# Kernel tuning notes

Hardware: AMD Instinct MI355X
Metric: run time of the kernel (lower is better)

The kernel has to match this reference:

```python
import jax, jax.numpy as jnp
import numpy as np

TAU = 1.2  # relaxed-categorical temperature (forward default)


def setup_inputs() -> dict:
    key = jax.random.key(0)
    ks = jax.random.split(key, 8)
    B, F, V, E, H, T = 1024, 2048, 4096, 256, 1024, 32
    n = lambda k, shape: jax.random.normal(k, shape, jnp.float32) * 0.1
    return {
        "t": jax.random.normal(ks[0], (B, F), jnp.float32),
        "embedding": n(ks[1], (V, E)),
        "aff_w": n(ks[2], (H, F)),
        "aff_b": jnp.zeros((H,), jnp.float32),
        "w_ih": n(ks[3], (4 * H, E)),
        "w_hh": n(ks[4], (4 * H, H)),
        "b_ih": jnp.zeros((4 * H,), jnp.float32),
        # PyTorch init: forget-gate bias (second quarter) set to 1
        "b_hh": jnp.zeros((4 * H,), jnp.float32).at[H:2 * H].set(1.0),
        "lp_w": n(ks[5], (V, H)),
        "lp_b": jnp.zeros((V,), jnp.float32),
        "start_token_idx": 1,
        "max_sentence_length": T,
    }


def reference(t, embedding, aff_w, aff_b, w_ih, w_hh, b_ih, b_hh, lp_w, lp_b,
              start_token_idx, max_sentence_length):
    B = t.shape[0]
    H = aff_w.shape[0]
    V = embedding.shape[0]

    h0 = t @ aff_w.T + aff_b                      # [B, H]
    c0 = jnp.zeros((B, H), t.dtype)
    tok0 = jax.nn.one_hot(jnp.full((B,), start_token_idx), V, dtype=t.dtype)

    # Gumbel noise for RelaxedOneHotCategorical rsample, one slab per step
    gumbel = jax.random.gumbel(jax.random.key(42), (max_sentence_length, B, V), t.dtype)

    def step(carry, g):
        h, c, tok = carry
        emb = tok @ embedding                     # [B, E] (one-hot/relaxed matmul)
        gates = emb @ w_ih.T + b_ih + h @ w_hh.T + b_hh  # [B, 4H]
        i, f, gg, o = jnp.split(gates, 4, axis=-1)        # PyTorch gate order i,f,g,o
        c = jax.nn.sigmoid(f) * c + jax.nn.sigmoid(i) * jnp.tanh(gg)
        h = jax.nn.sigmoid(o) * jnp.tanh(c)
        # softmax probs -> relaxed sample: softmax((log p + G)/tau)
        logp = jax.nn.log_softmax(h @ lp_w.T + lp_b, axis=-1)  # [B, V]
        y = jax.nn.softmax((logp + g) / TAU, axis=-1)
        hard = jax.nn.one_hot(jnp.argmax(y, axis=-1), V, dtype=y.dtype)
        tok = jax.lax.stop_gradient(hard - y) + y  # straight-through
        return (h, c, tok), tok

    _, toks = jax.lax.scan(step, (h0, c0, tok0), gumbel)  # toks: [T, B, V]
    message = jnp.concatenate([tok0[None], toks], axis=0)  # [T+1, B, V]
    return jnp.transpose(message, (1, 0, 2))               # [B, T+1, V]
```

## Files before the change

kernel.cpp:

```cpp
#include <hip/hip_runtime.h>
#include <math.h>


typedef _Float16 f16;
typedef f16 f16x8 __attribute__((ext_vector_type(8)));
typedef float f32x4 __attribute__((ext_vector_type(4)));

#define F16_MIN_NORM 6.104e-5f

__device__ __forceinline__ void split_f16(float v, f16& h, f16& l) {
  f16 h0 = (fabsf(v) < F16_MIN_NORM) ? (f16)0.0f : (f16)v;
  float r = (v - (float)h0) * 4096.0f;
  h = h0; l = (f16)r;
}

__device__ __forceinline__ float sigm(float x) { return 1.0f / (1.0f + expf(-x)); }

#define GLOAD_LDS16(gsrc, ldst)                                               \
  __builtin_amdgcn_global_load_lds(                                           \
      (const __attribute__((address_space(1))) unsigned int*)(const void*)(gsrc), \
      (__attribute__((address_space(3))) unsigned int*)(void*)(ldst), 16, 0, 0)


__device__ __forceinline__ unsigned tf_rotl(unsigned x, int r) {
  return (x << r) | (x >> (32 - r));
}

__device__ inline float gumbel_at(unsigned idx) {
  const unsigned ks0 = 0u;
  const unsigned ks1 = 42u;
  const unsigned ks2 = 0x1BD11BDAu ^ ks0 ^ ks1;
  unsigned x0 = 0u + ks0;
  unsigned x1 = idx + ks1;
#define TFR(rot) { x0 += x1; x1 = tf_rotl(x1, rot); x1 ^= x0; }
  TFR(13) TFR(15) TFR(26) TFR(6)
  x0 += ks1; x1 += ks2 + 1u;
  TFR(17) TFR(29) TFR(16) TFR(24)
  x0 += ks2; x1 += ks0 + 2u;
  TFR(13) TFR(15) TFR(26) TFR(6)
  x0 += ks0; x1 += ks1 + 3u;
  TFR(17) TFR(29) TFR(16) TFR(24)
  x0 += ks1; x1 += ks2 + 4u;
  TFR(13) TFR(15) TFR(26) TFR(6)
  x0 += ks2; x1 += ks0 + 5u;
#undef TFR
  const unsigned bits = x0 ^ x1;
  const float f = __uint_as_float((bits >> 9) | 0x3F800000u) - 1.0f;
  const float tiny = 1.17549435082228751e-38f;
  const float u = fmaxf(tiny, f * (1.0f - tiny) + tiny);
  return -logf(-logf(u));
}


__global__ void init_kernel(float* __restrict__ out, const int* __restrict__ startp,
                            int* __restrict__ tok, int Tp1, int V) {
  const int b = blockIdx.x;
  const int start = *startp;
  if (threadIdx.x == 0) tok[b] = start;
  float* orow = out + (size_t)b * Tp1 * V;
  const int tq = start >> 2;
  for (int v4 = threadIdx.x; v4 < V / 4; v4 += blockDim.x) {
    float4 v = make_float4(0.f, 0.f, 0.f, 0.f);
    if (v4 == tq) ((float*)&v)[start & 3] = 1.0f;
    ((float4*)orow)[v4] = v;
  }
}

__global__ void pack_gates_kernel(const float* __restrict__ wih,
                                  const float* __restrict__ whh,
                                  f16* __restrict__ w0, f16* __restrict__ w1,
                                  int E, int H, int K) {
  const int k = blockIdx.x * blockDim.x + threadIdx.x;
  const int p = blockIdx.y;
  if (k >= K) return;
  const int n = ((p >> 4) & 3) * H + ((p >> 6) << 4) + (p & 15);
  const float v = (k < E) ? wih[(size_t)n * E + k] : whh[(size_t)n * H + (k - E)];
  f16 h, l; split_f16(v, h, l);
  w0[(size_t)p * K + k] = h;
  w1[(size_t)p * K + k] = l;
}

__global__ void pack_bias_kernel(const float* __restrict__ bih,
                                 const float* __restrict__ bhh,
                                 float* __restrict__ bi, float* __restrict__ bh, int H) {
  const int p = blockIdx.x * blockDim.x + threadIdx.x;
  const int n = ((p >> 4) & 3) * H + ((p >> 6) << 4) + (p & 15);
  bi[p] = bih[n];
  bh[p] = bhh[n];
}

__global__ void split_kernel(const float* __restrict__ in,
                             f16* __restrict__ o0, f16* __restrict__ o1, int n) {
  const int i = blockIdx.x * blockDim.x + threadIdx.x;
  if (i < n) { f16 h, l; split_f16(in[i], h, l); o0[i] = h; o1[i] = l; }
}


__device__ __forceinline__ void stage_chunk(
    int chunk, int srow, int scol,
    const f16* __restrict__ a0s, const f16* __restrict__ a1s, int lda, int ka, int bm,
    const f16* __restrict__ b0s, const f16* __restrict__ b1s, int ldb, int kb, int bn,
    f16 (*ldsA0)[32], f16 (*ldsA1)[32], f16 (*ldsB0)[32], f16 (*ldsB1)[32])
{
  if (chunk < 8) {
    GLOAD_LDS16(a0s + (size_t)(bm + chunk * 16 + srow) * lda + ka + scol,
                &ldsA0[chunk * 16][0]);
  } else if (chunk < 16) {
    const int s = chunk - 8;
    GLOAD_LDS16(a1s + (size_t)(bm + s * 16 + srow) * lda + ka + scol,
                &ldsA1[s * 16][0]);
  } else if (chunk < 24) {
    const int s = chunk - 16;
    GLOAD_LDS16(b0s + (size_t)(bn + s * 16 + srow) * ldb + kb + scol,
                &ldsB0[s * 16][0]);
  } else {
    const int s = chunk - 24;
    GLOAD_LDS16(b1s + (size_t)(bn + s * 16 + srow) * ldb + kb + scol,
                &ldsB1[s * 16][0]);
  }
}

#define MFMA_DECLS                                                            \
  const int tid  = threadIdx.x;                                               \
  const int lane = tid & 63;                                                  \
  const int wid  = tid >> 6;                                                  \
  const int bm   = blockIdx.y * 128;                                          \
  const int bn   = blockIdx.x * 128;                                          \
  const int wm   = (wid & 3) * 32;                                            \
  const int wn   = (wid >> 2) * 64;                                           \
  const int fr   = lane & 15;                                                 \
  const int fk   = (((lane >> 4) ^ ((lane >> 1) & 3)) * 8);                   \
  const int srow = lane >> 2;                                                 \
  const int scol = (((lane & 3) ^ ((lane >> 3) & 3)) * 8);                    \
  f32x4 acc0[2][4], acc1[2][4];                                               \
  _Pragma("unroll") for (int i = 0; i < 2; ++i)                               \
  _Pragma("unroll") for (int j = 0; j < 4; ++j) {                             \
    acc0[i][j] = (f32x4)0.0f; acc1[i][j] = (f32x4)0.0f; }

#define MFMA_LDS_DECL                                                         \
  __shared__ f16 ldsA0[4][128][32], ldsA1[4][128][32],                        \
                 ldsB0[4][128][32], ldsB1[4][128][32];

#define MFMA_STAGE_TO(buf, a0s, a1s, lda, ka, b0s, b1s, ldb, kb)              \
  { _Pragma("unroll") for (int c = 0; c < 4; ++c)                             \
      stage_chunk(wid * 4 + c, srow, scol, (a0s), (a1s), (lda), (ka), bm,     \
                  (b0s), (b1s), (ldb), (kb), bn,                              \
                  ldsA0[(buf)], ldsA1[(buf)], ldsB0[(buf)], ldsB1[(buf)]); }

#define MFMA_COMPUTE_FROM(buf)                                                \
  {                                                                           \
    f16x8 a0[2], a1[2], b0[4], b1[4];                                         \
    _Pragma("unroll") for (int i = 0; i < 2; ++i) {                           \
      a0[i] = *(const f16x8*)&ldsA0[(buf)][wm + i * 16 + fr][fk];             \
      a1[i] = *(const f16x8*)&ldsA1[(buf)][wm + i * 16 + fr][fk];             \
    }                                                                         \
    _Pragma("unroll") for (int j = 0; j < 4; ++j) {                           \
      b0[j] = *(const f16x8*)&ldsB0[(buf)][wn + j * 16 + fr][fk];             \
      b1[j] = *(const f16x8*)&ldsB1[(buf)][wn + j * 16 + fr][fk];             \
    }                                                                         \
    _Pragma("unroll") for (int i = 0; i < 2; ++i)                             \
    _Pragma("unroll") for (int j = 0; j < 4; ++j) {                           \
      acc0[i][j] = __builtin_amdgcn_mfma_f32_16x16x32_f16(a0[i], b0[j], acc0[i][j], 0, 0, 0); \
      acc1[i][j] = __builtin_amdgcn_mfma_f32_16x16x32_f16(a0[i], b1[j], acc1[i][j], 0, 0, 0); \
      acc1[i][j] = __builtin_amdgcn_mfma_f32_16x16x32_f16(a1[i], b0[j], acc1[i][j], 0, 0, 0); \
    }                                                                         \
  }

#define PIPE_ITER(buf, DOSTAGE, VM)                                           \
  asm volatile("s_waitcnt vmcnt(" #VM ")" ::: "memory");                      \
  __builtin_amdgcn_s_barrier();                                               \
  asm volatile("" ::: "memory");                                              \
  DOSTAGE                                                                     \
  asm volatile("" ::: "memory");                                              \
  __builtin_amdgcn_s_setprio(1);                                              \
  MFMA_COMPUTE_FROM(buf)                                                      \
  __builtin_amdgcn_s_setprio(0);                                              \
  asm volatile("" ::: "memory");

#define PIPE(NT)                                                              \
  STAGE_T(0, 0) STAGE_T(1, 1) STAGE_T(2, 2)                                   \
  {                                                                           \
    int tt = 0;                                                               \
    for (; tt + 4 < (NT); tt += 4) {                                          \
      PIPE_ITER(0, STAGE_T(3, tt + 3), 8)                                     \
      PIPE_ITER(1, STAGE_T(0, tt + 4), 8)                                     \
      PIPE_ITER(2, STAGE_T(1, tt + 5), 8)                                     \
      PIPE_ITER(3, STAGE_T(2, tt + 6), 8)                                     \
    }                                                                         \
    PIPE_ITER(0, STAGE_T(3, tt + 3), 8)                                       \
    PIPE_ITER(1, {}, 8)                                                       \
    PIPE_ITER(2, {}, 4)                                                       \
    PIPE_ITER(3, {}, 0)                                                       \
  }

__global__ __launch_bounds__(512, 2) void h0_kernel(
    const f16* __restrict__ t0, const f16* __restrict__ t1, int F,
    const f16* __restrict__ aw0, const f16* __restrict__ aw1,
    const float* __restrict__ affb,
    f16* __restrict__ h0p, f16* __restrict__ h1p, int H,
    float* __restrict__ czero)
{
  MFMA_LDS_DECL
  MFMA_DECLS
  const int NT = F / 32;
#define STAGE_T(buf, t) MFMA_STAGE_TO(buf, t0, t1, F, (t) * 32, aw0, aw1, F, (t) * 32)
  PIPE(NT)
#undef STAGE_T
  const int q4 = (lane >> 4) * 4;
  const float s12 = 1.0f / 4096.0f;
  const int cn0 = bn + wn;
#pragma unroll
  for (int j = 0; j < 4; ++j) {
    const int col = cn0 + j * 16 + fr;
    const float bb = affb[col];
#pragma unroll
    for (int i = 0; i < 2; ++i) {
#pragma unroll
      for (int r = 0; r < 4; ++r) {
        const int row = bm + wm + i * 16 + q4 + r;
        const float v = (acc0[i][j][r] + acc1[i][j][r] * s12) + bb;
        f16 hh, hl; split_f16(v, hh, hl);
        const size_t off = (size_t)row * H + col;
        h0p[off] = hh; h1p[off] = hl;
        czero[off] = 0.0f;
      }
    }
  }
}

__global__ __launch_bounds__(512, 2) void gih_kernel(
    const f16* __restrict__ e0, const f16* __restrict__ e1, int E,
    const f16* __restrict__ w0, const f16* __restrict__ w1, int K,
    const float* __restrict__ bi, const float* __restrict__ bh,
    float* __restrict__ gih, int NP)
{
  MFMA_LDS_DECL
  MFMA_DECLS
  const int NT = E / 32;
#define STAGE_T(buf, t) MFMA_STAGE_TO(buf, e0, e1, E, (t) * 32, w0, w1, K, (t) * 32)
  PIPE(NT)
#undef STAGE_T
  const int q4 = (lane >> 4) * 4;
  const float s12 = 1.0f / 4096.0f;
  const int cn0 = bn + wn;
#pragma unroll
  for (int j = 0; j < 4; ++j) {
    const int col = cn0 + j * 16 + fr;
    const float bb = bi[col] + bh[col];
#pragma unroll
    for (int i = 0; i < 2; ++i)
#pragma unroll
      for (int r = 0; r < 4; ++r) {
        const int row = bm + wm + i * 16 + q4 + r;
        gih[(size_t)row * NP + col] = (acc0[i][j][r] + acc1[i][j][r] * s12) + bb;
      }
  }
}

__global__ __launch_bounds__(512, 2) void gates_kernel(
    const f16* __restrict__ hin0, const f16* __restrict__ hin1, int H,
    const f16* __restrict__ w0, const f16* __restrict__ w1, int K, int E,
    const float* __restrict__ gih, int NP, const int* __restrict__ tok,
    float* __restrict__ cbuf,
    f16* __restrict__ hout0, f16* __restrict__ hout1)
{
  MFMA_LDS_DECL
  MFMA_DECLS
  const int NT = H / 32;
#define STAGE_T(buf, t) MFMA_STAGE_TO(buf, hin0, hin1, H, (t) * 32, w0, w1, K, E + (t) * 32)
  PIPE(NT)
#undef STAGE_T
  const int q4 = (lane >> 4) * 4;
  const float s12 = 1.0f / 4096.0f;
  const int cn0 = bn + wn;
  const int nunit = (cn0 >> 2) + fr;
#pragma unroll
  for (int i = 0; i < 2; ++i) {
#pragma unroll
    for (int r = 0; r < 4; ++r) {
      const int row = bm + wm + i * 16 + q4 + r;
      const float* gr = gih + (size_t)tok[row] * NP + cn0 + fr;
      float gv[4];
#pragma unroll
      for (int j = 0; j < 4; ++j)
        gv[j] = (acc0[i][j][r] + acc1[i][j][r] * s12) + gr[j * 16];
      const size_t off = (size_t)row * H + nunit;
      const float c = cbuf[off];
      const float cn = __fadd_rn(__fmul_rn(sigm(gv[1]), c),
                                 __fmul_rn(sigm(gv[0]), tanhf(gv[2])));
      const float hn = __fmul_rn(sigm(gv[3]), tanhf(cn));
      cbuf[off] = cn;
      f16 hh, hl; split_f16(hn, hh, hl);
      hout0[off] = hh; hout1[off] = hl;
    }
  }
}

__global__ __launch_bounds__(512, 2) void logits_kernel(
    const f16* __restrict__ h0p, const f16* __restrict__ h1p, int H,
    const f16* __restrict__ w0, const f16* __restrict__ w1,
    const float* __restrict__ lpb,
    float* __restrict__ partM, int* __restrict__ partI,
    int step, int B, int V)
{
  MFMA_LDS_DECL
  MFMA_DECLS
  const int NT = H / 32;
#define STAGE_T(buf, t) MFMA_STAGE_TO(buf, h0p, h1p, H, (t) * 32, w0, w1, H, (t) * 32)
  PIPE(NT)
#undef STAGE_T
  const int q4 = (lane >> 4) * 4;
  const float s12 = 1.0f / 4096.0f;
  const int cn0 = bn + wn;
  float bv[4];
#pragma unroll
  for (int j = 0; j < 4; ++j) bv[j] = lpb[cn0 + j * 16 + fr];
#pragma unroll
  for (int i = 0; i < 2; ++i)
#pragma unroll
    for (int j = 0; j < 4; ++j) {
      const int col = cn0 + j * 16 + fr;
#pragma unroll
      for (int r = 0; r < 4; ++r) {
        const int row = bm + wm + i * 16 + q4 + r;
        const float logit = (acc0[i][j][r] + acc1[i][j][r] * s12) + bv[j];
        const unsigned gidx = ((unsigned)(step * B + row)) * (unsigned)V + (unsigned)col;
        acc0[i][j][r] = logit + gumbel_at(gidx);
      }
    }
  const int grp = cn0 >> 6;
#pragma unroll
  for (int i = 0; i < 2; ++i) {
#pragma unroll
    for (int r = 0; r < 4; ++r) {
      float mx = -INFINITY; int ix = 0;
#pragma unroll
      for (int j = 0; j < 4; ++j) {
        const float w = acc0[i][j][r];
        const int col = cn0 + j * 16 + fr;
        if (w > mx) { mx = w; ix = col; }
      }
#pragma unroll
      for (int m = 1; m < 16; m <<= 1) {
        const float om = __shfl_xor(mx, m, 64);
        const int oi = __shfl_xor(ix, m, 64);
        if (om > mx || (om == mx && oi < ix)) { mx = om; ix = oi; }
      }
      if (fr == 0) {
        const int row = bm + wm + i * 16 + q4 + r;
        partM[(size_t)row * 64 + grp] = mx;
        partI[(size_t)row * 64 + grp] = ix;
      }
    }
  }
}

__global__ __launch_bounds__(256) void finalize_kernel(
    const float* __restrict__ partM, const int* __restrict__ partI,
    float* __restrict__ out, int* __restrict__ tok,
    int step, int Tp1, int V)
{
  const int b = blockIdx.x;
  const int tid = threadIdx.x;
  __shared__ int s_tok;

  if (tid < 64) {
    float mx = partM[(size_t)b * 64 + tid];
    int ix = partI[(size_t)b * 64 + tid];
#pragma unroll
    for (int m = 1; m < 64; m <<= 1) {
      const float om = __shfl_xor(mx, m, 64);
      const int oi = __shfl_xor(ix, m, 64);
      if (om > mx || (om == mx && oi < ix)) { mx = om; ix = oi; }
    }
    if (tid == 0) { s_tok = ix; tok[b] = ix; }
  }
  __syncthreads();
  const int tk = s_tok;

  float* orow = out + ((size_t)b * Tp1 + step + 1) * V;
  const int tq = tk >> 2;
#pragma unroll
  for (int j = 0; j < 4; ++j) {
    const int idx = tid + 256 * j;
    float4 v = make_float4(0.f, 0.f, 0.f, 0.f);
    if (idx == tq) ((float*)&v)[tk & 3] = 1.0f;
    ((float4*)orow)[idx] = v;
  }
}


extern "C" void kernel_launch(void* const* d_in, const int* in_sizes, int n_in,
                              void* d_out, int out_size, void* d_ws, size_t ws_size,
                              hipStream_t stream) {
  const float* t     = (const float*)d_in[0];
  const float* emb   = (const float*)d_in[1];
  const float* affw  = (const float*)d_in[2];
  const float* affb  = (const float*)d_in[3];
  const float* wih   = (const float*)d_in[4];
  const float* whh   = (const float*)d_in[5];
  const float* bih   = (const float*)d_in[6];
  const float* bhh   = (const float*)d_in[7];
  const float* lpw   = (const float*)d_in[8];
  const float* lpb   = (const float*)d_in[9];
  const int*   start = (const int*)d_in[10];
  float* out = (float*)d_out;

  const int H = in_sizes[3];
  const int V = in_sizes[9];
  const int E = in_sizes[1] / V;
  const int F = in_sizes[2] / H;
  const int B = in_sizes[0] / F;
  const int Tp1 = out_size / (B * V);
  const int T = Tp1 - 1;
  const int KG = E + H;
  const int NP = 4 * H;

  char* p = (char*)d_ws;
  float* gihb  = (float*)p; p += (size_t)V * NP * 4;
  float* cbuf  = (float*)p; p += (size_t)B * H * 4;
  f16* hA0[2]; f16* hA1[2];
  hA0[0] = (f16*)p; p += (size_t)B * H * 2;
  hA1[0] = (f16*)p; p += (size_t)B * H * 2;
  hA0[1] = (f16*)p; p += (size_t)B * H * 2;
  hA1[1] = (f16*)p; p += (size_t)B * H * 2;
  f16* wg0 = (f16*)p; p += (size_t)V * KG * 2;
  f16* wg1 = (f16*)p; p += (size_t)V * KG * 2;
  f16* wl0 = (f16*)p; p += (size_t)V * H * 2;
  f16* wl1 = (f16*)p; p += (size_t)V * H * 2;
  f16* t0  = (f16*)p; p += (size_t)B * F * 2;
  f16* t1  = (f16*)p; p += (size_t)B * F * 2;
  f16* aw0 = (f16*)p; p += (size_t)H * F * 2;
  f16* aw1 = (f16*)p; p += (size_t)H * F * 2;
  f16* em0 = (f16*)p; p += (size_t)V * E * 2;
  f16* em1 = (f16*)p; p += (size_t)V * E * 2;
  float* bgi = (float*)p; p += (size_t)NP * 4;
  float* bgh = (float*)p; p += (size_t)NP * 4;
  float* partM = (float*)p; p += (size_t)B * 64 * 4;
  int*   partI = (int*)p;   p += (size_t)B * 64 * 4;
  int*   tokb  = (int*)p;   p += (size_t)B * 4;
  (void)ws_size; (void)n_in;

  init_kernel<<<B, 256, 0, stream>>>(out, start, tokb, Tp1, V);
  pack_gates_kernel<<<dim3((KG + 255) / 256, NP), 256, 0, stream>>>(
      wih, whh, wg0, wg1, E, H, KG);
  pack_bias_kernel<<<NP / 256, 256, 0, stream>>>(bih, bhh, bgi, bgh, H);
  split_kernel<<<(V * H + 255) / 256, 256, 0, stream>>>(lpw, wl0, wl1, V * H);
  split_kernel<<<(B * F + 255) / 256, 256, 0, stream>>>(t, t0, t1, B * F);
  split_kernel<<<(H * F + 255) / 256, 256, 0, stream>>>(affw, aw0, aw1, H * F);
  split_kernel<<<(V * E + 255) / 256, 256, 0, stream>>>(emb, em0, em1, V * E);
  h0_kernel<<<dim3(H / 128, B / 128), 512, 0, stream>>>(
      t0, t1, F, aw0, aw1, affb, hA0[0], hA1[0], H, cbuf);
  gih_kernel<<<dim3(NP / 128, V / 128), 512, 0, stream>>>(
      em0, em1, E, wg0, wg1, KG, bgi, bgh, gihb, NP);

  for (int s = 0; s < T; ++s) {
    const int cur = s & 1, nxt = (s + 1) & 1;
    gates_kernel<<<dim3(NP / 128, B / 128), 512, 0, stream>>>(
        hA0[cur], hA1[cur], H, wg0, wg1, KG, E, gihb, NP, tokb,
        cbuf, hA0[nxt], hA1[nxt]);
    logits_kernel<<<dim3(V / 128, B / 128), 512, 0, stream>>>(
        hA0[nxt], hA1[nxt], H, wl0, wl1, lpb,
        partM, partI, s, B, V);
    finalize_kernel<<<B, 256, 0, stream>>>(
        partM, partI, out, tokb, s, Tp1, V);
  }
}
```

Measured before the change: 3.779 ms.

## Load B operand directly into registers and swizzle block order for L2 reuse

The weight (B) operand no longer goes through LDS. Each wave loads its B fragments from global memory straight into double-buffered registers one k-chunk ahead, and only the A operand is still staged in LDS with async global-to-LDS loads. The block index is also remapped into groups of 8 columns to improve L2 locality. This halves LDS traffic and LDS footprint, possibly raising occupancy. In exchange it adds register pressure, and the B loads are uncoalesced per-lane 16-byte reads whose latency must be hidden by the register double-buffering.

```diff
diff --git a/kernel.cpp b/kernel.cpp
--- a/kernel.cpp
+++ b/kernel.cpp
@@ -96,101 +96,109 @@
 }
 
 
-__device__ __forceinline__ void stage_chunk(
-    int chunk, int srow, int scol,
-    const f16* __restrict__ a0s, const f16* __restrict__ a1s, int lda, int ka, int bm,
-    const f16* __restrict__ b0s, const f16* __restrict__ b1s, int ldb, int kb, int bn,
-    f16 (*ldsA0)[32], f16 (*ldsA1)[32], f16 (*ldsB0)[32], f16 (*ldsB1)[32])
-{
-  if (chunk < 8) {
-    GLOAD_LDS16(a0s + (size_t)(bm + chunk * 16 + srow) * lda + ka + scol,
-                &ldsA0[chunk * 16][0]);
-  } else if (chunk < 16) {
-    const int s = chunk - 8;
-    GLOAD_LDS16(a1s + (size_t)(bm + s * 16 + srow) * lda + ka + scol,
-                &ldsA1[s * 16][0]);
-  } else if (chunk < 24) {
-    const int s = chunk - 16;
-    GLOAD_LDS16(b0s + (size_t)(bn + s * 16 + srow) * ldb + kb + scol,
-                &ldsB0[s * 16][0]);
-  } else {
-    const int s = chunk - 24;
-    GLOAD_LDS16(b1s + (size_t)(bn + s * 16 + srow) * ldb + kb + scol,
-                &ldsB1[s * 16][0]);
-  }
-}
-
 #define MFMA_DECLS                                                            \
   const int tid  = threadIdx.x;                                               \
   const int lane = tid & 63;                                                  \
   const int wid  = tid >> 6;                                                  \
-  const int bm   = blockIdx.y * 128;                                          \
-  const int bn   = blockIdx.x * 128;                                          \
+  const int nx_  = gridDim.x;                                                 \
+  const int lin_ = blockIdx.x + blockIdx.y * nx_;                             \
+  const int nx8_ = nx_ >> 3;                                                  \
+  const int sh_  = (nx8_ == 4) ? 2 : ((nx8_ == 2) ? 1 : 0);                   \
+  const int bx_  = (lin_ & 7) * nx8_ + ((lin_ >> 3) & (nx8_ - 1));            \
+  const int by_  = (lin_ >> 3) >> sh_;                                        \
+  const int bm   = by_ * 128;                                                 \
+  const int bn   = bx_ * 128;                                                 \
   const int wm   = (wid & 3) * 32;                                            \
   const int wn   = (wid >> 2) * 64;                                           \
   const int fr   = lane & 15;                                                 \
   const int fk   = (((lane >> 4) ^ ((lane >> 1) & 3)) * 8);                   \
   const int srow = lane >> 2;                                                 \
   const int scol = (((lane & 3) ^ ((lane >> 3) & 3)) * 8);                    \
+  f16x8 br0[2][4], br1[2][4];                                                 \
   f32x4 acc0[2][4], acc1[2][4];                                               \
   _Pragma("unroll") for (int i = 0; i < 2; ++i)                               \
   _Pragma("unroll") for (int j = 0; j < 4; ++j) {                             \
     acc0[i][j] = (f32x4)0.0f; acc1[i][j] = (f32x4)0.0f; }
 
 #define MFMA_LDS_DECL                                                         \
-  __shared__ f16 ldsA0[4][128][32], ldsA1[4][128][32],                        \
-                 ldsB0[4][128][32], ldsB1[4][128][32];
-
-#define MFMA_STAGE_TO(buf, a0s, a1s, lda, ka, b0s, b1s, ldb, kb)              \
-  { _Pragma("unroll") for (int c = 0; c < 4; ++c)                             \
-      stage_chunk(wid * 4 + c, srow, scol, (a0s), (a1s), (lda), (ka), bm,     \
-                  (b0s), (b1s), (ldb), (kb), bn,                              \
-                  ldsA0[(buf)], ldsA1[(buf)], ldsB0[(buf)], ldsB1[(buf)]); }
-
-#define MFMA_COMPUTE_FROM(buf)                                                \
+  __shared__ f16 ldsA0[4][128][32], ldsA1[4][128][32];
+
+#define MFMA_BP_DECL(Bsrc0, Bsrc1, ldb, kb0)                                  \
+  const f16* bp0[4]; const f16* bp1[4];                                       \
+  _Pragma("unroll") for (int j = 0; j < 4; ++j) {                             \
+    const int brow = bn + wn + j * 16 + fr;                                   \
+    bp0[j] = (Bsrc0) + (size_t)brow * (ldb) + (kb0) + (lane >> 4) * 8;        \
+    bp1[j] = (Bsrc1) + (size_t)brow * (ldb) + (kb0) + (lane >> 4) * 8;        \
+  }
+
+#define LOADB_C(set, c)                                                       \
+  { _Pragma("unroll") for (int j = 0; j < 4; ++j) {                           \
+      br0[set][j] = *(const f16x8*)(bp0[j] + (c) * 32);                       \
+      br1[set][j] = *(const f16x8*)(bp1[j] + (c) * 32);                       \
+    } }
+
+#define BUMPB                                                                 \
+  { _Pragma("unroll") for (int j = 0; j < 4; ++j) {                           \
+      bp0[j] += 128; bp1[j] += 128;                                           \
+    } }
+
+#define MFMA_STAGE_A(buf, a0s, a1s, lda, ka)                                  \
+  { const int ch_ = wid * 2;                                                  \
+    if (ch_ < 8) {                                                            \
+      GLOAD_LDS16((a0s) + (size_t)(bm + ch_ * 16 + srow) * (lda) + (ka) + scol,      \
+                  &ldsA0[(buf)][ch_ * 16][0]);                                \
+      GLOAD_LDS16((a0s) + (size_t)(bm + (ch_ + 1) * 16 + srow) * (lda) + (ka) + scol,\
+                  &ldsA0[(buf)][(ch_ + 1) * 16][0]);                          \
+    } else {                                                                  \
+      GLOAD_LDS16((a1s) + (size_t)(bm + (ch_ - 8) * 16 + srow) * (lda) + (ka) + scol,\
+                  &ldsA1[(buf)][(ch_ - 8) * 16][0]);                          \
+      GLOAD_LDS16((a1s) + (size_t)(bm + (ch_ - 7) * 16 + srow) * (lda) + (ka) + scol,\
+                  &ldsA1[(buf)][(ch_ - 7) * 16][0]);                          \
+    } }
+
+#define MFMA_COMPUTE_FROM(buf, set)                                           \
   {                                                                           \
-    f16x8 a0[2], a1[2], b0[4], b1[4];                                         \
+    f16x8 a0[2], a1[2];                                                       \
     _Pragma("unroll") for (int i = 0; i < 2; ++i) {                           \
       a0[i] = *(const f16x8*)&ldsA0[(buf)][wm + i * 16 + fr][fk];             \
       a1[i] = *(const f16x8*)&ldsA1[(buf)][wm + i * 16 + fr][fk];             \
     }                                                                         \
-    _Pragma("unroll") for (int j = 0; j < 4; ++j) {                           \
-      b0[j] = *(const f16x8*)&ldsB0[(buf)][wn + j * 16 + fr][fk];             \
-      b1[j] = *(const f16x8*)&ldsB1[(buf)][wn + j * 16 + fr][fk];             \
-    }                                                                         \
     _Pragma("unroll") for (int i = 0; i < 2; ++i)                             \
     _Pragma("unroll") for (int j = 0; j < 4; ++j) {                           \
-      acc0[i][j] = __builtin_amdgcn_mfma_f32_16x16x32_f16(a0[i], b0[j], acc0[i][j], 0, 0, 0); \
-      acc1[i][j] = __builtin_amdgcn_mfma_f32_16x16x32_f16(a0[i], b1[j], acc1[i][j], 0, 0, 0); \
-      acc1[i][j] = __builtin_amdgcn_mfma_f32_16x16x32_f16(a1[i], b0[j], acc1[i][j], 0, 0, 0); \
+      acc0[i][j] = __builtin_amdgcn_mfma_f32_16x16x32_f16(a0[i], br0[set][j], acc0[i][j], 0, 0, 0); \
+      acc1[i][j] = __builtin_amdgcn_mfma_f32_16x16x32_f16(a0[i], br1[set][j], acc1[i][j], 0, 0, 0); \
+      acc1[i][j] = __builtin_amdgcn_mfma_f32_16x16x32_f16(a1[i], br0[set][j], acc1[i][j], 0, 0, 0); \
     }                                                                         \
   }
 
-#define PIPE_ITER(buf, DOSTAGE, VM)                                           \
+#define PIPE_ITER(bufc, set, VM, DO_B, DO_A)                                  \
   asm volatile("s_waitcnt vmcnt(" #VM ")" ::: "memory");                      \
   __builtin_amdgcn_s_barrier();                                               \
   asm volatile("" ::: "memory");                                              \
-  DOSTAGE                                                                     \
-  asm volatile("" ::: "memory");                                              \
+  DO_B                                                                        \
+  DO_A                                                                        \
   __builtin_amdgcn_s_setprio(1);                                              \
-  MFMA_COMPUTE_FROM(buf)                                                      \
+  MFMA_COMPUTE_FROM(bufc, set)                                                \
   __builtin_amdgcn_s_setprio(0);                                              \
   asm volatile("" ::: "memory");
 
 #define PIPE(NT)                                                              \
-  STAGE_T(0, 0) STAGE_T(1, 1) STAGE_T(2, 2)                                   \
+  STAGE_T(0, 0) STAGE_T(1, 1)                                                 \
+  LOADB_C(0, 0)                                                               \
+  STAGE_T(2, 2)                                                               \
   {                                                                           \
     int tt = 0;                                                               \
-    for (; tt + 4 < (NT); tt += 4) {                                          \
-      PIPE_ITER(0, STAGE_T(3, tt + 3), 8)                                     \
-      PIPE_ITER(1, STAGE_T(0, tt + 4), 8)                                     \
-      PIPE_ITER(2, STAGE_T(1, tt + 5), 8)                                     \
-      PIPE_ITER(3, STAGE_T(2, tt + 6), 8)                                     \
+    for (; tt < (NT) - 4; tt += 4) {                                          \
+      PIPE_ITER(0, 0, 12, LOADB_C(1, 1), STAGE_T(3, tt + 3))                  \
+      PIPE_ITER(1, 1, 12, LOADB_C(0, 2), STAGE_T(0, tt + 4))                  \
+      PIPE_ITER(2, 0, 12, LOADB_C(1, 3), STAGE_T(1, tt + 5))                  \
+      PIPE_ITER(3, 1, 12, LOADB_C(0, 4), STAGE_T(2, tt + 6))                  \
+      BUMPB                                                                   \
     }                                                                         \
-    PIPE_ITER(0, STAGE_T(3, tt + 3), 8)                                       \
-    PIPE_ITER(1, {}, 8)                                                       \
-    PIPE_ITER(2, {}, 4)                                                       \
-    PIPE_ITER(3, {}, 0)                                                       \
+    PIPE_ITER(0, 0, 12, LOADB_C(1, 1), STAGE_T(3, tt + 3))                    \
+    PIPE_ITER(1, 1, 12, LOADB_C(0, 2), {})                                    \
+    PIPE_ITER(2, 0, 10, LOADB_C(1, 3), {})                                    \
+    PIPE_ITER(3, 1, 8, {}, {})                                                \
   }
 
 __global__ __launch_bounds__(512, 2) void h0_kernel(
@@ -202,8 +210,9 @@
 {
   MFMA_LDS_DECL
   MFMA_DECLS
+  MFMA_BP_DECL(aw0, aw1, F, 0)
   const int NT = F / 32;
-#define STAGE_T(buf, t) MFMA_STAGE_TO(buf, t0, t1, F, (t) * 32, aw0, aw1, F, (t) * 32)
+#define STAGE_T(buf, t) MFMA_STAGE_A(buf, t0, t1, F, (t) * 32)
   PIPE(NT)
 #undef STAGE_T
   const int q4 = (lane >> 4) * 4;
@@ -236,8 +245,9 @@
 {
   MFMA_LDS_DECL
   MFMA_DECLS
+  MFMA_BP_DECL(w0, w1, K, 0)
   const int NT = E / 32;
-#define STAGE_T(buf, t) MFMA_STAGE_TO(buf, e0, e1, E, (t) * 32, w0, w1, K, (t) * 32)
+#define STAGE_T(buf, t) MFMA_STAGE_A(buf, e0, e1, E, (t) * 32)
   PIPE(NT)
 #undef STAGE_T
   const int q4 = (lane >> 4) * 4;
@@ -266,8 +276,9 @@
 {
   MFMA_LDS_DECL
   MFMA_DECLS
+  MFMA_BP_DECL(w0, w1, K, E)
   const int NT = H / 32;
-#define STAGE_T(buf, t) MFMA_STAGE_TO(buf, hin0, hin1, H, (t) * 32, w0, w1, K, E + (t) * 32)
+#define STAGE_T(buf, t) MFMA_STAGE_A(buf, hin0, hin1, H, (t) * 32)
   PIPE(NT)
 #undef STAGE_T
   const int q4 = (lane >> 4) * 4;
@@ -305,8 +316,9 @@
 {
   MFMA_LDS_DECL
   MFMA_DECLS
+  MFMA_BP_DECL(w0, w1, H, 0)
   const int NT = H / 32;
-#define STAGE_T(buf, t) MFMA_STAGE_TO(buf, h0p, h1p, H, (t) * 32, w0, w1, H, (t) * 32)
+#define STAGE_T(buf, t) MFMA_STAGE_A(buf, h0p, h1p, H, (t) * 32)
   PIPE(NT)
 #undef STAGE_T
   const int q4 = (lane >> 4) * 4;
```

After: 6.847 ms. +81.2%, slower.

## Use 4-wave 64x64 warp tiles with double-buffered LDS pipeline

Applied to the files above, without the earlier changes.

Switches the shared MFMA GEMM template from 8 waves with 32x64 warp tiles to 4 waves with 64x64 warp tiles. Each wave now stages one full operand plane. The 4-deep LDS ring with partial vmcnt waits becomes a 2-buffer ping-pong that waits for all loads before each barrier. The goal is more register-level reuse of A/B fragments, less LDS traffic per MFMA and half the LDS footprint, which could allow more blocks per CU. The cost is fewer waves to hide latency, a full vmcnt(0) stall every k-step, and heavier register pressure from 32 accumulators per wave.

```diff
diff --git a/kernel.cpp b/kernel.cpp
--- a/kernel.cpp
+++ b/kernel.cpp
@@ -96,61 +96,50 @@
 }
 
 
-__device__ __forceinline__ void stage_chunk(
-    int chunk, int srow, int scol,
-    const f16* __restrict__ a0s, const f16* __restrict__ a1s, int lda, int ka, int bm,
-    const f16* __restrict__ b0s, const f16* __restrict__ b1s, int ldb, int kb, int bn,
-    f16 (*ldsA0)[32], f16 (*ldsA1)[32], f16 (*ldsB0)[32], f16 (*ldsB1)[32])
-{
-  if (chunk < 8) {
-    GLOAD_LDS16(a0s + (size_t)(bm + chunk * 16 + srow) * lda + ka + scol,
-                &ldsA0[chunk * 16][0]);
-  } else if (chunk < 16) {
-    const int s = chunk - 8;
-    GLOAD_LDS16(a1s + (size_t)(bm + s * 16 + srow) * lda + ka + scol,
-                &ldsA1[s * 16][0]);
-  } else if (chunk < 24) {
-    const int s = chunk - 16;
-    GLOAD_LDS16(b0s + (size_t)(bn + s * 16 + srow) * ldb + kb + scol,
-                &ldsB0[s * 16][0]);
-  } else {
-    const int s = chunk - 24;
-    GLOAD_LDS16(b1s + (size_t)(bn + s * 16 + srow) * ldb + kb + scol,
-                &ldsB1[s * 16][0]);
-  }
-}
-
 #define MFMA_DECLS                                                            \
   const int tid  = threadIdx.x;                                               \
   const int lane = tid & 63;                                                  \
   const int wid  = tid >> 6;                                                  \
   const int bm   = blockIdx.y * 128;                                          \
   const int bn   = blockIdx.x * 128;                                          \
-  const int wm   = (wid & 3) * 32;                                            \
-  const int wn   = (wid >> 2) * 64;                                           \
+  const int wm   = (wid & 1) * 64;                                            \
+  const int wn   = (wid >> 1) * 64;                                           \
   const int fr   = lane & 15;                                                 \
   const int fk   = (((lane >> 4) ^ ((lane >> 1) & 3)) * 8);                   \
   const int srow = lane >> 2;                                                 \
   const int scol = (((lane & 3) ^ ((lane >> 3) & 3)) * 8);                    \
-  f32x4 acc0[2][4], acc1[2][4];                                               \
-  _Pragma("unroll") for (int i = 0; i < 2; ++i)                               \
+  f32x4 acc0[4][4], acc1[4][4];                                               \
+  _Pragma("unroll") for (int i = 0; i < 4; ++i)                               \
   _Pragma("unroll") for (int j = 0; j < 4; ++j) {                             \
     acc0[i][j] = (f32x4)0.0f; acc1[i][j] = (f32x4)0.0f; }
 
 #define MFMA_LDS_DECL                                                         \
-  __shared__ f16 ldsA0[4][128][32], ldsA1[4][128][32],                        \
-                 ldsB0[4][128][32], ldsB1[4][128][32];
+  __shared__ f16 ldsA0[2][128][32], ldsA1[2][128][32],                        \
+                 ldsB0[2][128][32], ldsB1[2][128][32];
 
 #define MFMA_STAGE_TO(buf, a0s, a1s, lda, ka, b0s, b1s, ldb, kb)              \
-  { _Pragma("unroll") for (int c = 0; c < 4; ++c)                             \
-      stage_chunk(wid * 4 + c, srow, scol, (a0s), (a1s), (lda), (ka), bm,     \
-                  (b0s), (b1s), (ldb), (kb), bn,                              \
-                  ldsA0[(buf)], ldsA1[(buf)], ldsB0[(buf)], ldsB1[(buf)]); }
+  { if (wid == 0) {                                                           \
+      _Pragma("unroll") for (int c = 0; c < 8; ++c)                           \
+        GLOAD_LDS16((a0s) + (size_t)(bm + c * 16 + srow) * (lda) + (ka) + scol, \
+                    &ldsA0[(buf)][c * 16][0]);                                \
+    } else if (wid == 1) {                                                    \
+      _Pragma("unroll") for (int c = 0; c < 8; ++c)                           \
+        GLOAD_LDS16((a1s) + (size_t)(bm + c * 16 + srow) * (lda) + (ka) + scol, \
+                    &ldsA1[(buf)][c * 16][0]);                                \
+    } else if (wid == 2) {                                                    \
+      _Pragma("unroll") for (int c = 0; c < 8; ++c)                           \
+        GLOAD_LDS16((b0s) + (size_t)(bn + c * 16 + srow) * (ldb) + (kb) + scol, \
+                    &ldsB0[(buf)][c * 16][0]);                                \
+    } else {                                                                  \
+      _Pragma("unroll") for (int c = 0; c < 8; ++c)                           \
+        GLOAD_LDS16((b1s) + (size_t)(bn + c * 16 + srow) * (ldb) + (kb) + scol, \
+                    &ldsB1[(buf)][c * 16][0]);                                \
+    } }
 
 #define MFMA_COMPUTE_FROM(buf)                                                \
   {                                                                           \
-    f16x8 a0[2], a1[2], b0[4], b1[4];                                         \
-    _Pragma("unroll") for (int i = 0; i < 2; ++i) {                           \
+    f16x8 a0[4], a1[4], b0[4], b1[4];                                         \
+    _Pragma("unroll") for (int i = 0; i < 4; ++i) {                           \
       a0[i] = *(const f16x8*)&ldsA0[(buf)][wm + i * 16 + fr][fk];             \
       a1[i] = *(const f16x8*)&ldsA1[(buf)][wm + i * 16 + fr][fk];             \
     }                                                                         \
@@ -158,7 +147,7 @@
       b0[j] = *(const f16x8*)&ldsB0[(buf)][wn + j * 16 + fr][fk];             \
       b1[j] = *(const f16x8*)&ldsB1[(buf)][wn + j * 16 + fr][fk];             \
     }                                                                         \
-    _Pragma("unroll") for (int i = 0; i < 2; ++i)                             \
+    _Pragma("unroll") for (int i = 0; i < 4; ++i)                             \
     _Pragma("unroll") for (int j = 0; j < 4; ++j) {                           \
       acc0[i][j] = __builtin_amdgcn_mfma_f32_16x16x32_f16(a0[i], b0[j], acc0[i][j], 0, 0, 0); \
       acc1[i][j] = __builtin_amdgcn_mfma_f32_16x16x32_f16(a0[i], b1[j], acc1[i][j], 0, 0, 0); \
@@ -166,34 +155,25 @@
     }                                                                         \
   }
 
-#define PIPE_ITER(buf, DOSTAGE, VM)                                           \
-  asm volatile("s_waitcnt vmcnt(" #VM ")" ::: "memory");                      \
+#define PIPE_ITER(bufc, bufs, DO_STAGE)                                       \
+  asm volatile("s_waitcnt vmcnt(0)" ::: "memory");                            \
   __builtin_amdgcn_s_barrier();                                               \
   asm volatile("" ::: "memory");                                              \
-  DOSTAGE                                                                     \
+  DO_STAGE                                                                    \
   asm volatile("" ::: "memory");                                              \
   __builtin_amdgcn_s_setprio(1);                                              \
-  MFMA_COMPUTE_FROM(buf)                                                      \
+  MFMA_COMPUTE_FROM(bufc)                                                     \
   __builtin_amdgcn_s_setprio(0);                                              \
   asm volatile("" ::: "memory");
 
 #define PIPE(NT)                                                              \
-  STAGE_T(0, 0) STAGE_T(1, 1) STAGE_T(2, 2)                                   \
-  {                                                                           \
-    int tt = 0;                                                               \
-    for (; tt + 4 < (NT); tt += 4) {                                          \
-      PIPE_ITER(0, STAGE_T(3, tt + 3), 8)                                     \
-      PIPE_ITER(1, STAGE_T(0, tt + 4), 8)                                     \
-      PIPE_ITER(2, STAGE_T(1, tt + 5), 8)                                     \
-      PIPE_ITER(3, STAGE_T(2, tt + 6), 8)                                     \
-    }                                                                         \
-    PIPE_ITER(0, STAGE_T(3, tt + 3), 8)                                       \
-    PIPE_ITER(1, {}, 8)                                                       \
-    PIPE_ITER(2, {}, 4)                                                       \
-    PIPE_ITER(3, {}, 0)                                                       \
-  }
-
-__global__ __launch_bounds__(512, 2) void h0_kernel(
+  STAGE_T(0, 0)                                                               \
+  for (int tt = 0; tt < (NT); tt += 2) {                                      \
+    PIPE_ITER(0, 1, if (tt + 1 < (NT)) { STAGE_T(1, tt + 1) })                \
+    PIPE_ITER(1, 0, if (tt + 2 < (NT)) { STAGE_T(0, tt + 2) })                \
+  }
+
+__global__ __launch_bounds__(256, 2) void h0_kernel(
     const f16* __restrict__ t0, const f16* __restrict__ t1, int F,
     const f16* __restrict__ aw0, const f16* __restrict__ aw1,
     const float* __restrict__ affb,
@@ -214,7 +194,7 @@
     const int col = cn0 + j * 16 + fr;
     const float bb = affb[col];
 #pragma unroll
-    for (int i = 0; i < 2; ++i) {
+    for (int i = 0; i < 4; ++i) {
 #pragma unroll
       for (int r = 0; r < 4; ++r) {
         const int row = bm + wm + i * 16 + q4 + r;
@@ -228,7 +208,7 @@
   }
 }
 
-__global__ __launch_bounds__(512, 2) void gih_kernel(
+__global__ __launch_bounds__(256, 2) void gih_kernel(
     const f16* __restrict__ e0, const f16* __restrict__ e1, int E,
     const f16* __restrict__ w0, const f16* __restrict__ w1, int K,
     const float* __restrict__ bi, const float* __restrict__ bh,
@@ -248,7 +228,7 @@
     const int col = cn0 + j * 16 + fr;
     const float bb = bi[col] + bh[col];
 #pragma unroll
-    for (int i = 0; i < 2; ++i)
+    for (int i = 0; i < 4; ++i)
 #pragma unroll
       for (int r = 0; r < 4; ++r) {
         const int row = bm + wm + i * 16 + q4 + r;
@@ -257,7 +237,7 @@
   }
 }
 
-__global__ __launch_bounds__(512, 2) void gates_kernel(
+__global__ __launch_bounds__(256, 2) void gates_kernel(
     const f16* __restrict__ hin0, const f16* __restrict__ hin1, int H,
     const f16* __restrict__ w0, const f16* __restrict__ w1, int K, int E,
     const float* __restrict__ gih, int NP, const int* __restrict__ tok,
@@ -275,7 +255,7 @@
   const int cn0 = bn + wn;
   const int nunit = (cn0 >> 2) + fr;
 #pragma unroll
-  for (int i = 0; i < 2; ++i) {
+  for (int i = 0; i < 4; ++i) {
 #pragma unroll
     for (int r = 0; r < 4; ++r) {
       const int row = bm + wm + i * 16 + q4 + r;
@@ -296,7 +276,7 @@
   }
 }
 
-__global__ __launch_bounds__(512, 2) void logits_kernel(
+__global__ __launch_bounds__(256, 2) void logits_kernel(
     const f16* __restrict__ h0p, const f16* __restrict__ h1p, int H,
     const f16* __restrict__ w0, const f16* __restrict__ w1,
     const float* __restrict__ lpb,
@@ -316,7 +296,7 @@
 #pragma unroll
   for (int j = 0; j < 4; ++j) bv[j] = lpb[cn0 + j * 16 + fr];
 #pragma unroll
-  for (int i = 0; i < 2; ++i)
+  for (int i = 0; i < 4; ++i)
 #pragma unroll
     for (int j = 0; j < 4; ++j) {
       const int col = cn0 + j * 16 + fr;
@@ -330,7 +310,7 @@
     }
   const int grp = cn0 >> 6;
 #pragma unroll
-  for (int i = 0; i < 2; ++i) {
+  for (int i = 0; i < 4; ++i) {
 #pragma unroll
     for (int r = 0; r < 4; ++r) {
       float mx = -INFINITY; int ix = 0;
@@ -449,17 +429,17 @@
   split_kernel<<<(B * F + 255) / 256, 256, 0, stream>>>(t, t0, t1, B * F);
   split_kernel<<<(H * F + 255) / 256, 256, 0, stream>>>(affw, aw0, aw1, H * F);
   split_kernel<<<(V * E + 255) / 256, 256, 0, stream>>>(emb, em0, em1, V * E);
-  h0_kernel<<<dim3(H / 128, B / 128), 512, 0, stream>>>(
+  h0_kernel<<<dim3(H / 128, B / 128), 256, 0, stream>>>(
       t0, t1, F, aw0, aw1, affb, hA0[0], hA1[0], H, cbuf);
-  gih_kernel<<<dim3(NP / 128, V / 128), 512, 0, stream>>>(
+  gih_kernel<<<dim3(NP / 128, V / 128), 256, 0, stream>>>(
       em0, em1, E, wg0, wg1, KG, bgi, bgh, gihb, NP);
 
   for (int s = 0; s < T; ++s) {
     const int cur = s & 1, nxt = (s + 1) & 1;
-    gates_kernel<<<dim3(NP / 128, B / 128), 512, 0, stream>>>(
+    gates_kernel<<<dim3(NP / 128, B / 128), 256, 0, stream>>>(
         hA0[cur], hA1[cur], H, wg0, wg1, KG, E, gihb, NP, tokb,
         cbuf, hA0[nxt], hA1[nxt]);
-    logits_kernel<<<dim3(V / 128, B / 128), 512, 0, stream>>>(
+    logits_kernel<<<dim3(V / 128, B / 128), 256, 0, stream>>>(
         hA0[nxt], hA1[nxt], H, wl0, wl1, lpb,
         partM, partI, s, B, V);
     finalize_kernel<<<B, 256, 0, stream>>>(
```

Result: slower. 4.125 ms (+9.2%).

## Fuse token finalize into gates kernel and widen MFMA pipeline window

Applied to the files above, without the earlier changes.

Removes the per-step finalize kernel launch. Each gates block now reduces the previous step's partial argmax (partM/partI) for its 128 rows, writes its 128-column slice of the one-hot output row, and uses the token from shared memory for the gih gather. A single finalize launch remains after the loop for the last step. The software pipeline is also restructured to stage two K-tiles per barrier and compute two buffers per wait with vmcnt(0). This trades deeper load/compute overlap for fewer barriers, and adds redundant argmax reductions across the NP/128 column blocks.

```diff
diff --git a/kernel.cpp b/kernel.cpp
--- a/kernel.cpp
+++ b/kernel.cpp
@@ -166,32 +166,29 @@
     }                                                                         \
   }
 
-#define PIPE_ITER(buf, DOSTAGE, VM)                                           \
-  asm volatile("s_waitcnt vmcnt(" #VM ")" ::: "memory");                      \
+#define PIPE_WINDOW(bufA, bufB, DO_STAGE_PAIR)                                \
+  asm volatile("s_waitcnt vmcnt(0)" ::: "memory");                            \
   __builtin_amdgcn_s_barrier();                                               \
   asm volatile("" ::: "memory");                                              \
-  DOSTAGE                                                                     \
+  DO_STAGE_PAIR                                                               \
   asm volatile("" ::: "memory");                                              \
   __builtin_amdgcn_s_setprio(1);                                              \
-  MFMA_COMPUTE_FROM(buf)                                                      \
+  MFMA_COMPUTE_FROM(bufA)                                                     \
+  MFMA_COMPUTE_FROM(bufB)                                                     \
   __builtin_amdgcn_s_setprio(0);                                              \
   asm volatile("" ::: "memory");
 
-#define PIPE(NT)                                                              \
-  STAGE_T(0, 0) STAGE_T(1, 1) STAGE_T(2, 2)                                   \
-  {                                                                           \
-    int tt = 0;                                                               \
-    for (; tt + 4 < (NT); tt += 4) {                                          \
-      PIPE_ITER(0, STAGE_T(3, tt + 3), 8)                                     \
-      PIPE_ITER(1, STAGE_T(0, tt + 4), 8)                                     \
-      PIPE_ITER(2, STAGE_T(1, tt + 5), 8)                                     \
-      PIPE_ITER(3, STAGE_T(2, tt + 6), 8)                                     \
-    }                                                                         \
-    PIPE_ITER(0, STAGE_T(3, tt + 3), 8)                                       \
-    PIPE_ITER(1, {}, 8)                                                       \
-    PIPE_ITER(2, {}, 4)                                                       \
-    PIPE_ITER(3, {}, 0)                                                       \
-  }
+#define PIPE_PROLOGUE  STAGE_T(0, 0) STAGE_T(1, 1)
+
+#define PIPE_BODY(NT)                                                         \
+  for (int tt = 0; tt < (NT); tt += 4) {                                      \
+    PIPE_WINDOW(0, 1,                                                         \
+      if (tt + 2 < (NT)) { STAGE_T(2, tt + 2) STAGE_T(3, tt + 3) })           \
+    PIPE_WINDOW(2, 3,                                                         \
+      if (tt + 4 < (NT)) { STAGE_T(0, tt + 4) STAGE_T(1, tt + 5) })           \
+  }
+
+#define PIPE(NT) PIPE_PROLOGUE PIPE_BODY(NT)
 
 __global__ __launch_bounds__(512, 2) void h0_kernel(
     const f16* __restrict__ t0, const f16* __restrict__ t1, int F,
@@ -260,15 +257,50 @@
 __global__ __launch_bounds__(512, 2) void gates_kernel(
     const f16* __restrict__ hin0, const f16* __restrict__ hin1, int H,
     const f16* __restrict__ w0, const f16* __restrict__ w1, int K, int E,
-    const float* __restrict__ gih, int NP, const int* __restrict__ tok,
+    const float* __restrict__ gih, int NP, const int* __restrict__ tokb,
+    const float* __restrict__ partM, const int* __restrict__ partI,
+    float* __restrict__ out, int step, int Tp1, int V,
     float* __restrict__ cbuf,
     f16* __restrict__ hout0, f16* __restrict__ hout1)
 {
   MFMA_LDS_DECL
+  __shared__ int s_tok2[128];
   MFMA_DECLS
   const int NT = H / 32;
 #define STAGE_T(buf, t) MFMA_STAGE_TO(buf, hin0, hin1, H, (t) * 32, w0, w1, K, E + (t) * 32)
-  PIPE(NT)
+  PIPE_PROLOGUE
+  if (step == 0) {
+    for (int r = tid; r < 128; r += 512) s_tok2[r] = tokb[bm + r];
+  } else {
+    const int rloc = wid * 16 + (lane >> 2);
+    const int row = bm + rloc;
+    const int g0 = (lane & 3) * 16;
+    float mx = -INFINITY; int ix = 0;
+#pragma unroll
+    for (int g = 0; g < 16; ++g) {
+      const float om = partM[(size_t)row * 64 + g0 + g];
+      const int oi = partI[(size_t)row * 64 + g0 + g];
+      if (om > mx || (om == mx && oi < ix)) { mx = om; ix = oi; }
+    }
+#pragma unroll
+    for (int m = 1; m < 4; m <<= 1) {
+      const float om = __shfl_xor(mx, m, 64);
+      const int oi = __shfl_xor(ix, m, 64);
+      if (om > mx || (om == mx && oi < ix)) { mx = om; ix = oi; }
+    }
+    if ((lane & 3) == 0) s_tok2[rloc] = ix;
+    float* orow = out + ((size_t)row * Tp1 + step) * V + bn;
+    const int tl = ix - bn;
+    const int tq = tl >> 2;
+#pragma unroll
+    for (int k = 0; k < 8; ++k) {
+      const int c4 = (lane & 3) * 8 + k;
+      float4 v = make_float4(0.f, 0.f, 0.f, 0.f);
+      if ((unsigned)tl < 128u && c4 == tq) ((float*)&v)[tl & 3] = 1.0f;
+      ((float4*)orow)[c4] = v;
+    }
+  }
+  PIPE_BODY(NT)
 #undef STAGE_T
   const int q4 = (lane >> 4) * 4;
   const float s12 = 1.0f / 4096.0f;
@@ -278,8 +310,9 @@
   for (int i = 0; i < 2; ++i) {
 #pragma unroll
     for (int r = 0; r < 4; ++r) {
-      const int row = bm + wm + i * 16 + q4 + r;
-      const float* gr = gih + (size_t)tok[row] * NP + cn0 + fr;
+      const int rl = wm + i * 16 + q4 + r;
+      const int row = bm + rl;
+      const float* gr = gih + (size_t)s_tok2[rl] * NP + cn0 + fr;
       float gv[4];
 #pragma unroll
       for (int j = 0; j < 4; ++j)
@@ -458,11 +491,12 @@
     const int cur = s & 1, nxt = (s + 1) & 1;
     gates_kernel<<<dim3(NP / 128, B / 128), 512, 0, stream>>>(
         hA0[cur], hA1[cur], H, wg0, wg1, KG, E, gihb, NP, tokb,
+        partM, partI, out, s, Tp1, V,
         cbuf, hA0[nxt], hA1[nxt]);
     logits_kernel<<<dim3(V / 128, B / 128), 512, 0, stream>>>(
         hA0[nxt], hA1[nxt], H, wl0, wl1, lpb,
         partM, partI, s, B, V);
-    finalize_kernel<<<B, 256, 0, stream>>>(
-        partM, partI, out, tokb, s, Tp1, V);
-  }
-}
+  }
+  finalize_kernel<<<B, 256, 0, stream>>>(
+      partM, partI, out, tokb, T - 1, Tp1, V);
+}
```

Measured after the change: 3.904 ms. +3.3%, slower.
